# Performance work log

Hardware: AMD Instinct MI355X
Metric: run time of the kernel (lower is better)

Reference implementation:

```python
import jax, jax.numpy as jnp
import numpy as np

B, T, INPUT_DIM = 32, 256, 512
VQ_DIM = 128
NUM_EMBED = 8192
CODEBOOK_NUM = 1
SPLIT_NUM = 4
FREQ = INPUT_DIM // 2 + 1  # 257


def setup_inputs() -> dict:
    key = jax.random.key(0)
    k1, k2, k3, k4 = jax.random.split(key, 4)
    x = jax.random.normal(k1, (B, T, INPUT_DIM), dtype=jnp.float32)
    # xavier_normal_ on (input_dim, vq_dim): std = sqrt(2/(fan_in+fan_out))
    xav_std = float(np.sqrt(2.0 / (INPUT_DIM + VQ_DIM)))
    projector = jax.random.normal(k2, (INPUT_DIM, VQ_DIM), dtype=jnp.float32) * xav_std
    codebook = jax.random.normal(k3, (CODEBOOK_NUM, NUM_EMBED, VQ_DIM), dtype=jnp.float32)
    random_matrix = jax.random.randint(k4, (FREQ,), 0, SPLIT_NUM, dtype=jnp.int32)
    return {"x": x, "projector": projector, "codebook": codebook,
            "random_matrix": random_matrix}


def reference(x, projector, codebook, random_matrix):
    n = x.shape[-1]
    x_fft = jnp.fft.rfft(x, axis=-1)                              # [B,T,F] complex
    # masks[s, f] = (random_matrix[f] == s); vectorizes the per-split list
    masks = (random_matrix[None, :] == jnp.arange(SPLIT_NUM)[:, None])  # [S,F] bool
    x_sub = x_fft[:, :, None, :] * masks                           # [B,T,S,F]
    x_recon = jnp.fft.irfft(x_sub, n=n, axis=-1)                   # [B,T,S,n]
    feat = jnp.einsum('btns,sd->btnd', x_recon, projector)         # [B,T,S,D]
    feat = feat / jnp.linalg.norm(feat, axis=-1, keepdims=True)
    cb = codebook / jnp.linalg.norm(codebook, axis=-1, keepdims=True)  # [C,M,D]
    sim = jnp.einsum('btnd,cmd->btncm', feat, cb)                  # [B,T,S,C,M]
    return jnp.argmax(sim, axis=-1)                                # [B,T,S,C]
```

## Files before the change

### kernel.cpp

```cpp
#include <hip/hip_runtime.h>
#include <math.h>

#define BT 8192
#define NDIM 512
#define NFREQ 257
#define DDIM 128
#define NEMBED 8192
#define NQ 4
#define ROWS 32768

typedef _Float16 half8 __attribute__((ext_vector_type(8)));
typedef _Float16 half2v __attribute__((ext_vector_type(2)));
typedef float f32x4 __attribute__((ext_vector_type(4)));

#define SCALE_DN 2.44140625e-4f

__global__ __launch_bounds__(512) void build_K_kernel(const int* __restrict__ rm,
                                                      float* __restrict__ Kmat) {
    __shared__ float ctab[512];
    __shared__ int rms[NFREQ];
    int t = threadIdx.x;
    ctab[t] = cospif((float)t * (1.0f / 256.0f));
    if (t < NFREQ) rms[t] = rm[t];
    __syncthreads();
    float acc0 = 0.f, acc1 = 0.f, acc2 = 0.f, acc3 = 0.f;
    for (int f = 0; f < NFREQ; ++f) {
        float w = (f == 0 || f == 256) ? 1.0f : 2.0f;
        float c = w * ctab[(f * t) & 511];
        int s = rms[f];
        acc0 += (s == 0) ? c : 0.0f;
        acc1 += (s == 1) ? c : 0.0f;
        acc2 += (s == 2) ? c : 0.0f;
        acc3 += (s == 3) ? c : 0.0f;
    }
    const float sc = 1.0f / 512.0f;
    Kmat[0 * 512 + t] = acc0 * sc;
    Kmat[1 * 512 + t] = acc1 * sc;
    Kmat[2 * 512 + t] = acc2 * sc;
    Kmat[3 * 512 + t] = acc3 * sc;
}

__global__ __launch_bounds__(128) void build_W_split(const float* __restrict__ proj,
                                                     const float* __restrict__ Kmat,
                                                     _Float16* __restrict__ Wth,
                                                     _Float16* __restrict__ Wtl) {
    int nt = blockIdx.x, s = blockIdx.y, d = threadIdx.x;
    int n0 = nt * 8;
    __shared__ float Ks[512];
    for (int i = d; i < 512; i += 128) Ks[i] = Kmat[s * 512 + i];
    __syncthreads();
    float acc[8] = {};
    for (int p16 = 0; p16 < 512; p16 += 16) {
        float wv[23];
#pragma unroll
        for (int j2 = 0; j2 < 23; ++j2) wv[j2] = Ks[(p16 - n0 + j2 - 7) & 511];
#pragma unroll
        for (int j = 0; j < 16; ++j) {
            float xp = proj[(p16 + j) * DDIM + d];
#pragma unroll
            for (int i = 0; i < 8; ++i)
                acc[i] = fmaf(xp, wv[7 + j - i], acc[i]);
        }
    }
    size_t cbase = (size_t)(s * DDIM + d) * 512 + n0;
#pragma unroll
    for (int i = 0; i < 8; ++i) {
        float f = acc[i] * 256.0f;
        _Float16 h = (_Float16)f;
        Wth[cbase + i] = h;
        Wtl[cbase + i] = (_Float16)((f - (float)h) * 4096.0f);
    }
}

__global__ __launch_bounds__(256) void cbsplit_kernel(const float* __restrict__ cb,
                                                      _Float16* __restrict__ chi,
                                                      _Float16* __restrict__ clo) {
    int code = blockIdx.x * 4 + (threadIdx.x >> 6);
    int l = threadIdx.x & 63;
    float2 v = ((const float2*)(cb + (size_t)code * DDIM))[l];
    float ss = fmaf(v.x, v.x, v.y * v.y);
#pragma unroll
    for (int m = 32; m; m >>= 1) ss += __shfl_xor(ss, m);
    float r = 1.0f / sqrtf(ss);
    float a = v.x * r, b = v.y * r;
    _Float16 ha = (_Float16)a, hb = (_Float16)b;
    half2v hv = {ha, hb};
    half2v lv = {(_Float16)((a - (float)ha) * 4096.0f), (_Float16)((b - (float)hb) * 4096.0f)};
    int cr = code & 15, tile = code >> 4;
    int kt = l >> 4, lg = (l >> 2) & 3, j = 2 * (l & 3);
    size_t addr = (size_t)tile * 2048 + kt * 512 + lg * 128 + cr * 8 + j;
    *(half2v*)(chi + addr) = hv;
    *(half2v*)(clo + addr) = lv;
}

__global__ __launch_bounds__(256) void fused_feat(const float* __restrict__ x,
                                                  const _Float16* __restrict__ Wth,
                                                  const _Float16* __restrict__ Wtl,
                                                  _Float16* __restrict__ fhi,
                                                  _Float16* __restrict__ flo) {
    __shared__ __align__(16) char smem[59392];
    float* xs = (float*)smem;
    _Float16* Wh = (_Float16*)(smem + 18432);
    _Float16* Wl = (_Float16*)(smem + 38912);

    int t = threadIdx.x;
    int w = t >> 6, lr = t & 15, lg = (t >> 4) & 3;
    int row0 = blockIdx.x * 64;
    int sIdx = blockIdx.y;

    int xr_r = t >> 2, xr_c = (t & 3) * 8;
    int wcol = t >> 1, wh_h = t & 1;
    const float* xsrc = x + (size_t)(row0 + xr_r) * NDIM + xr_c;
    const _Float16* whsrc = Wth + (size_t)(sIdx * 128 + wcol) * 512 + wh_h * 16;
    const _Float16* wlsrc = Wtl + (size_t)(sIdx * 128 + wcol) * 512 + wh_h * 16;

    f32x4 c0[8], c1[8];
#pragma unroll
    for (int i = 0; i < 8; ++i) { c0[i] = (f32x4){0.f,0.f,0.f,0.f}; c1[i] = c0[i]; }

    {
        float4 a0 = *(const float4*)(xsrc);
        float4 a1 = *(const float4*)(xsrc + 4);
        *(float4*)&xs[xr_r * 36 + xr_c] = a0;
        *(float4*)&xs[xr_r * 36 + xr_c + 4] = a1;
        half8 h0 = *(const half8*)(whsrc);
        half8 h1 = *(const half8*)(whsrc + 8);
        half8 l0 = *(const half8*)(wlsrc);
        half8 l1 = *(const half8*)(wlsrc + 8);
        *(half8*)&Wh[wcol * 40 + wh_h * 16] = h0;
        *(half8*)&Wh[wcol * 40 + wh_h * 16 + 8] = h1;
        *(half8*)&Wl[wcol * 40 + wh_h * 16] = l0;
        *(half8*)&Wl[wcol * 40 + wh_h * 16 + 8] = l1;
    }

    for (int it = 0; it < 16; ++it) {
        __syncthreads();
        int buf = it & 1;
        float4 nx0, nx1; half8 nh0, nh1, nl0, nl1;
        bool have = (it + 1) < 16;
        if (have) {
            int k0 = (it + 1) * 32;
            nx0 = *(const float4*)(xsrc + k0);
            nx1 = *(const float4*)(xsrc + k0 + 4);
            nh0 = *(const half8*)(whsrc + k0);
            nh1 = *(const half8*)(whsrc + k0 + 8);
            nl0 = *(const half8*)(wlsrc + k0);
            nl1 = *(const half8*)(wlsrc + k0 + 8);
        }
        const float* xb = xs + buf * 2304;
        float4 f0 = *(const float4*)&xb[(w * 16 + lr) * 36 + lg * 8];
        float4 f1 = *(const float4*)&xb[(w * 16 + lr) * 36 + lg * 8 + 4];
        float fv[8] = {f0.x, f0.y, f0.z, f0.w, f1.x, f1.y, f1.z, f1.w};
        half8 ah, al;
#pragma unroll
        for (int j = 0; j < 8; ++j) {
            _Float16 h = (_Float16)fv[j];
            ah[j] = h;
            al[j] = (_Float16)((fv[j] - (float)h) * 4096.0f);
        }
        const _Float16* whb = Wh + buf * 5120;
        const _Float16* wlb = Wl + buf * 5120;
#pragma unroll
        for (int set = 0; set < 8; ++set) {
            int bcol = set * 16 + lr;
            half8 bh = *(const half8*)&whb[bcol * 40 + lg * 8];
            half8 bl = *(const half8*)&wlb[bcol * 40 + lg * 8];
            c0[set] = __builtin_amdgcn_mfma_f32_16x16x32_f16(ah, bh, c0[set], 0, 0, 0);
            c1[set] = __builtin_amdgcn_mfma_f32_16x16x32_f16(ah, bl, c1[set], 0, 0, 0);
            c1[set] = __builtin_amdgcn_mfma_f32_16x16x32_f16(al, bh, c1[set], 0, 0, 0);
        }
        __syncthreads();
        if (have) {
            *(float4*)&xs[(buf ^ 1) * 2304 + xr_r * 36 + xr_c] = nx0;
            *(float4*)&xs[(buf ^ 1) * 2304 + xr_r * 36 + xr_c + 4] = nx1;
            _Float16* dh = Wh + (buf ^ 1) * 5120 + wcol * 40 + wh_h * 16;
            _Float16* dl = Wl + (buf ^ 1) * 5120 + wcol * 40 + wh_h * 16;
            *(half8*)(dh) = nh0; *(half8*)(dh + 8) = nh1;
            *(half8*)(dl) = nl0; *(half8*)(dl + 8) = nl1;
        }
    }
    __syncthreads();

    float* few = (float*)smem + w * 2112;
    float ss[4] = {0.f, 0.f, 0.f, 0.f};
    float vv[8][4];
#pragma unroll
    for (int set = 0; set < 8; ++set)
#pragma unroll
        for (int r = 0; r < 4; ++r) {
            float v = fmaf(c1[set][r], SCALE_DN, c0[set][r]);
            vv[set][r] = v;
            ss[r] = fmaf(v, v, ss[r]);
        }
#pragma unroll
    for (int r = 0; r < 4; ++r) {
#pragma unroll
        for (int m = 1; m < 16; m <<= 1) ss[r] += __shfl_xor(ss[r], m);
    }
    float rn[4];
#pragma unroll
    for (int r = 0; r < 4; ++r) rn[r] = rsqrtf(ss[r]);
#pragma unroll
    for (int set = 0; set < 8; ++set)
#pragma unroll
        for (int r = 0; r < 4; ++r)
            few[(4 * lg + r) * 132 + set * 16 + lr] = vv[set][r] * rn[r];
    __syncthreads();
    int l = t & 63;
    int rr = l >> 2, q = l & 3;
    size_t btg = (size_t)(row0 + w * 16 + rr);
    size_t dst = (btg * 4 + sIdx) * DDIM + q * 32;
#pragma unroll
    for (int g = 0; g < 4; ++g) {
        half8 oh, ol;
#pragma unroll
        for (int j = 0; j < 8; ++j) {
            float f = few[rr * 132 + q * 32 + g * 8 + j];
            _Float16 h = (_Float16)f;
            oh[j] = h;
            ol[j] = (_Float16)((f - (float)h) * 4096.0f);
        }
        *(half8*)(fhi + dst + g * 8) = oh;
        *(half8*)(flo + dst + g * 8) = ol;
    }
}

__global__ __launch_bounds__(256, 2) void sim_argmax_part(const _Float16* __restrict__ fhi,
                                                          const _Float16* __restrict__ flo,
                                                          const _Float16* __restrict__ chi,
                                                          const _Float16* __restrict__ clo,
                                                          float* __restrict__ pv,
                                                          int* __restrict__ pi) {
    __shared__ float redv[256][17];
    __shared__ int   redi[256][17];

    int t = threadIdx.x;
    int w = t >> 6, l = t & 63, lr = t & 15, lg = (t >> 4) & 3;
    int row0 = blockIdx.x * 256;
    int q = blockIdx.y;

    half8 ahi[4][4], alo[4][4];
#pragma unroll
    for (int s = 0; s < 4; ++s)
#pragma unroll
        for (int kt = 0; kt < 4; ++kt) {
            size_t off = (size_t)(row0 + w * 64 + s * 16 + lr) * DDIM + kt * 32 + lg * 8;
            ahi[s][kt] = *(const half8*)(fhi + off);
            alo[s][kt] = *(const half8*)(flo + off);
        }

    const half8* cf = (const half8*)chi;
    const half8* cv = (const half8*)clo;
    size_t base = (size_t)(q * (NEMBED / NQ / 16)) * 256 + l;

    half8 bh[4], bl[4];
#pragma unroll
    for (int kt = 0; kt < 4; ++kt) {
        bh[kt] = cf[base + kt * 64];
        bl[kt] = cv[base + kt * 64];
    }

    float best[4][4];
    int btile[4][4];
#pragma unroll
    for (int s = 0; s < 4; ++s)
#pragma unroll
        for (int r = 0; r < 4; ++r) { best[s][r] = -1e30f; btile[s][r] = 0; }

    const int NT = NEMBED / (16 * NQ);
    for (int it = 0; it < NT; ++it) {
        f32x4 a0[4], a1[4];
#pragma unroll
        for (int s = 0; s < 4; ++s) { a0[s] = (f32x4){0.f,0.f,0.f,0.f}; a1[s] = a0[s]; }
        size_t nb = base + (size_t)(it + 1) * 256;
        bool have = (it + 1) < NT;
#pragma unroll
        for (int kt = 0; kt < 4; ++kt) {
#pragma unroll
            for (int s = 0; s < 4; ++s) {
                a0[s] = __builtin_amdgcn_mfma_f32_16x16x32_f16(ahi[s][kt], bh[kt], a0[s], 0, 0, 0);
                a1[s] = __builtin_amdgcn_mfma_f32_16x16x32_f16(ahi[s][kt], bl[kt], a1[s], 0, 0, 0);
                a1[s] = __builtin_amdgcn_mfma_f32_16x16x32_f16(alo[s][kt], bh[kt], a1[s], 0, 0, 0);
            }
            if (have) {
                bh[kt] = cf[nb + kt * 64];
                bl[kt] = cv[nb + kt * 64];
            }
        }
#pragma unroll
        for (int s = 0; s < 4; ++s)
#pragma unroll
            for (int r = 0; r < 4; ++r) {
                float v = fmaf(a1[s][r], SCALE_DN, a0[s][r]);
                if (v > best[s][r]) { best[s][r] = v; btile[s][r] = it; }
            }
    }

#pragma unroll
    for (int s = 0; s < 4; ++s)
#pragma unroll
        for (int r = 0; r < 4; ++r) {
            int row = w * 64 + s * 16 + 4 * lg + r;
            redv[row][lr] = best[s][r];
            redi[row][lr] = q * (NEMBED / NQ) + btile[s][r] * 16 + lr;
        }
    __syncthreads();
    {
        float bv = redv[t][0]; int bi = redi[t][0];
#pragma unroll
        for (int c = 1; c < 16; ++c) {
            float v = redv[t][c]; int ii = redi[t][c];
            if (v > bv || (v == bv && ii < bi)) { bv = v; bi = ii; }
        }
        pv[(size_t)q * ROWS + row0 + t] = bv;
        pi[(size_t)q * ROWS + row0 + t] = bi;
    }
}

__global__ __launch_bounds__(256) void merge_argmax(const float* __restrict__ pv,
                                                    const int* __restrict__ pi,
                                                    int* __restrict__ out) {
    int row = blockIdx.x * 256 + threadIdx.x;
    float bv = pv[row]; int bi = pi[row];
#pragma unroll
    for (int q = 1; q < NQ; ++q) {
        float v = pv[(size_t)q * ROWS + row];
        if (v > bv) { bv = v; bi = pi[(size_t)q * ROWS + row]; }
    }
    out[row] = bi;
}

extern "C" void kernel_launch(void* const* d_in, const int* in_sizes, int n_in,
                              void* d_out, int out_size, void* d_ws, size_t ws_size,
                              hipStream_t stream) {
    const float* x    = (const float*)d_in[0];
    const float* proj = (const float*)d_in[1];
    const float* cb   = (const float*)d_in[2];
    const int*   rm   = (const int*)d_in[3];
    int* out = (int*)d_out;

    char* wsb = (char*)d_ws;
    float*    Kmat = (float*)(wsb + 0);
    _Float16* Wth  = (_Float16*)(wsb + 8192);
    _Float16* Wtl  = (_Float16*)(wsb + 532480);
    _Float16* chi  = (_Float16*)(wsb + 1056768);
    _Float16* clo  = (_Float16*)(wsb + 3153920);
    _Float16* fhi  = (_Float16*)(wsb + 5251072);
    _Float16* flo  = (_Float16*)(wsb + 13639680);
    float*    pv   = (float*)(wsb + 22028288);
    int*      pi   = (int*)(wsb + 22552576);

    build_K_kernel<<<1, 512, 0, stream>>>(rm, Kmat);
    build_W_split<<<dim3(64, 4), 128, 0, stream>>>(proj, Kmat, Wth, Wtl);
    cbsplit_kernel<<<NEMBED / 4, 256, 0, stream>>>(cb, chi, clo);
    fused_feat<<<dim3(128, 4), 256, 0, stream>>>(x, Wth, Wtl, fhi, flo);
    sim_argmax_part<<<dim3(ROWS / 256, NQ), 256, 0, stream>>>(fhi, flo, chi, clo, pv, pi);
    merge_argmax<<<ROWS / 256, 256, 0, stream>>>(pv, pi, out);
}
```

Measured before the change: 285.0 us.

## Fold K-matrix build into W kernel, double codebook splits, raise sim occupancy

Drops the single-block build_K kernel and instead has each build_W_split block recompute its own split's K row in shared memory, which removes a serial one-block launch from the dependency chain but duplicates that cosine work across 64 blocks. Doubles the number of codebook partitions in the similarity/argmax stage so the grid has twice as many blocks, and raises the launch-bounds occupancy hint from 2 to 4 blocks per CU. The higher occupancy target can force register spills in the MFMA kernel, which holds large fragment arrays. The merge step now reads twice as many partial results.

```diff
diff --git a/kernel.cpp b/kernel.cpp
--- a/kernel.cpp
+++ b/kernel.cpp
@@ -6,7 +6,7 @@
 #define NFREQ 257
 #define DDIM 128
 #define NEMBED 8192
-#define NQ 4
+#define NQ 8
 #define ROWS 32768
 
 typedef _Float16 half8 __attribute__((ext_vector_type(8)));
@@ -15,39 +15,27 @@
 
 #define SCALE_DN 2.44140625e-4f
 
-__global__ __launch_bounds__(512) void build_K_kernel(const int* __restrict__ rm,
-                                                      float* __restrict__ Kmat) {
-    __shared__ float ctab[512];
-    __shared__ int rms[NFREQ];
-    int t = threadIdx.x;
-    ctab[t] = cospif((float)t * (1.0f / 256.0f));
-    if (t < NFREQ) rms[t] = rm[t];
-    __syncthreads();
-    float acc0 = 0.f, acc1 = 0.f, acc2 = 0.f, acc3 = 0.f;
-    for (int f = 0; f < NFREQ; ++f) {
-        float w = (f == 0 || f == 256) ? 1.0f : 2.0f;
-        float c = w * ctab[(f * t) & 511];
-        int s = rms[f];
-        acc0 += (s == 0) ? c : 0.0f;
-        acc1 += (s == 1) ? c : 0.0f;
-        acc2 += (s == 2) ? c : 0.0f;
-        acc3 += (s == 3) ? c : 0.0f;
-    }
-    const float sc = 1.0f / 512.0f;
-    Kmat[0 * 512 + t] = acc0 * sc;
-    Kmat[1 * 512 + t] = acc1 * sc;
-    Kmat[2 * 512 + t] = acc2 * sc;
-    Kmat[3 * 512 + t] = acc3 * sc;
-}
-
 __global__ __launch_bounds__(128) void build_W_split(const float* __restrict__ proj,
-                                                     const float* __restrict__ Kmat,
+                                                     const int* __restrict__ rm,
                                                      _Float16* __restrict__ Wth,
                                                      _Float16* __restrict__ Wtl) {
     int nt = blockIdx.x, s = blockIdx.y, d = threadIdx.x;
     int n0 = nt * 8;
+    __shared__ float ctab[512];
     __shared__ float Ks[512];
-    for (int i = d; i < 512; i += 128) Ks[i] = Kmat[s * 512 + i];
+    __shared__ int rms[NFREQ];
+    for (int i = d; i < 512; i += 128) ctab[i] = cospif((float)i * (1.0f / 256.0f));
+    for (int i = d; i < NFREQ; i += 128) rms[i] = rm[i];
+    __syncthreads();
+    for (int base = d; base < 512; base += 128) {
+        float acc = 0.0f;
+        for (int f = 0; f < NFREQ; ++f) {
+            float w = (f == 0 || f == 256) ? 1.0f : 2.0f;
+            float c = w * ctab[(f * base) & 511];
+            acc += (rms[f] == s) ? c : 0.0f;
+        }
+        Ks[base] = acc * (1.0f / 512.0f);
+    }
     __syncthreads();
     float acc[8] = {};
     for (int p16 = 0; p16 < 512; p16 += 16) {
@@ -225,7 +213,7 @@
     }
 }
 
-__global__ __launch_bounds__(256, 2) void sim_argmax_part(const _Float16* __restrict__ fhi,
+__global__ __launch_bounds__(256, 4) void sim_argmax_part(const _Float16* __restrict__ fhi,
                                                           const _Float16* __restrict__ flo,
                                                           const _Float16* __restrict__ chi,
                                                           const _Float16* __restrict__ clo,
@@ -340,18 +328,16 @@
     int* out = (int*)d_out;
 
     char* wsb = (char*)d_ws;
-    float*    Kmat = (float*)(wsb + 0);
-    _Float16* Wth  = (_Float16*)(wsb + 8192);
-    _Float16* Wtl  = (_Float16*)(wsb + 532480);
-    _Float16* chi  = (_Float16*)(wsb + 1056768);
-    _Float16* clo  = (_Float16*)(wsb + 3153920);
-    _Float16* fhi  = (_Float16*)(wsb + 5251072);
-    _Float16* flo  = (_Float16*)(wsb + 13639680);
-    float*    pv   = (float*)(wsb + 22028288);
-    int*      pi   = (int*)(wsb + 22552576);
-
-    build_K_kernel<<<1, 512, 0, stream>>>(rm, Kmat);
-    build_W_split<<<dim3(64, 4), 128, 0, stream>>>(proj, Kmat, Wth, Wtl);
+    _Float16* Wth  = (_Float16*)(wsb + 0);
+    _Float16* Wtl  = (_Float16*)(wsb + 524288);
+    _Float16* chi  = (_Float16*)(wsb + 1048576);
+    _Float16* clo  = (_Float16*)(wsb + 3145728);
+    _Float16* fhi  = (_Float16*)(wsb + 5242880);
+    _Float16* flo  = (_Float16*)(wsb + 13631488);
+    float*    pv   = (float*)(wsb + 22020096);
+    int*      pi   = (int*)(wsb + 23068672);
+
+    build_W_split<<<dim3(64, 4), 128, 0, stream>>>(proj, rm, Wth, Wtl);
     cbsplit_kernel<<<NEMBED / 4, 256, 0, stream>>>(cb, chi, clo);
     fused_feat<<<dim3(128, 4), 256, 0, stream>>>(x, Wth, Wtl, fhi, flo);
     sim_argmax_part<<<dim3(ROWS / 256, NQ), 256, 0, stream>>>(fhi, flo, chi, clo, pv, pi);
```

Measured after the change: 1.035 ms. 263% more time.
